# Kernel tuning notes

Measured on AMD Instinct MI355X. Metric: run time of the kernel, lower is better.

Reference implementation:

```python
import jax, jax.numpy as jnp
import numpy as np

B, N, F_IN, H, E = 8, 10000, 128, 128, 160000


def setup_inputs() -> dict:
    key = jax.random.key(0)
    ks = jax.random.split(key, 6)
    x = jax.random.normal(ks[0], (B, N, F_IN), dtype=jnp.float32)
    edge_index = jax.random.randint(ks[1], (2, E), 0, N, dtype=jnp.int64)
    # GCNConv params (glorot-ish scale), LayerNorm affine params
    W1 = jax.random.normal(ks[2], (F_IN, H), dtype=jnp.float32) / np.sqrt(F_IN)
    b1 = jnp.zeros((H,), dtype=jnp.float32)
    W2 = jax.random.normal(ks[3], (H, H), dtype=jnp.float32) / np.sqrt(H)
    b2 = jnp.zeros((H,), dtype=jnp.float32)
    ln_w = jnp.ones((H,), dtype=jnp.float32)
    ln_b = jnp.zeros((H,), dtype=jnp.float32)
    return {"x": x, "edge_index": edge_index, "W1": W1, "b1": b1,
            "W2": W2, "b2": b2, "ln_w": ln_w, "ln_b": ln_b}


def reference(x, edge_index, W1, b1, W2, b2, ln_w, ln_b):
    # x: [B, N, F]; edge_index: [2, E] shared across batch (tiled per graph
    # in the original via node offsets -> equivalent to vmapping over batch).
    n = x.shape[1]
    loops = jnp.arange(n, dtype=edge_index.dtype)
    src = jnp.concatenate([edge_index[0], loops])  # add self-loops (GCNConv default)
    dst = jnp.concatenate([edge_index[1], loops])
    # symmetric degree normalization: deg over targets with self-loops
    deg = jax.ops.segment_sum(jnp.ones(dst.shape[0], dtype=x.dtype), dst, num_segments=n)
    dinv = jnp.where(deg > 0, jax.lax.rsqrt(deg), 0.0)
    w_e = dinv[src] * dinv[dst]  # [E+N] per-edge norm

    def gcn_agg(h):  # h: [B, N, H] -> gather, scale, scatter-add
        msg = h[:, src, :] * w_e[None, :, None]  # [B, E+N, H]
        return jax.vmap(lambda m: jax.ops.segment_sum(m, dst, num_segments=n))(msg)

    h1 = jax.nn.relu(gcn_agg(x @ W1) + b1)
    h2 = gcn_agg(h1 @ W2) + b2
    # LayerNorm over last dim (eps=1e-5, torch default)
    mu = jnp.mean(h2, axis=-1, keepdims=True)
    var = jnp.mean(jnp.square(h2 - mu), axis=-1, keepdims=True)
    out = (h2 - mu) * jax.lax.rsqrt(var + 1e-5) * ln_w + ln_b
    return out  # [B, N, H]
```

## Files before the change

kernel.cpp:

```cpp
#include <hip/hip_runtime.h>
#include <hip/hip_bf16.h>

#define NNODES 10000
#define NB 8
#define NF 128
#define NE 160000

typedef __attribute__((ext_vector_type(8))) short  short8;
typedef __attribute__((ext_vector_type(8))) unsigned short ushort8;
typedef __attribute__((ext_vector_type(4))) float  f32x4;

__device__ __forceinline__ unsigned short f2b(float f) {
    union { float f; unsigned u; } v; v.f = f;
    unsigned r = v.u + 0x7FFF + ((v.u >> 16) & 1);
    return (unsigned short)(r >> 16);
}
__device__ __forceinline__ float b2f(unsigned short h) {
    union { unsigned u; float f; } v; v.u = ((unsigned)h) << 16;
    return v.f;
}


__global__ void k_zero(int* __restrict__ cnt, int* __restrict__ fill) {
    int i = blockIdx.x * blockDim.x + threadIdx.x;
    if (i < NNODES) { cnt[i] = 0; fill[i] = 0; }
}

__global__ void k_count(const int* __restrict__ ei, int* __restrict__ cnt) {
    int e = blockIdx.x * blockDim.x + threadIdx.x;
    if (e < NE) atomicAdd(&cnt[ei[NE + e]], 1);
}

__global__ void k_dinv(const int* __restrict__ cnt, float* __restrict__ dinv) {
    int i = blockIdx.x * blockDim.x + threadIdx.x;
    if (i < NNODES) dinv[i] = rsqrtf((float)(cnt[i] + 1));
}

__global__ void k_scan(const int* __restrict__ cnt, int* __restrict__ row_ptr) {
    __shared__ int part[1024];
    int t = threadIdx.x;
    const int CH = (NNODES + 1023) / 1024;
    int lo = t * CH, hi = min(lo + CH, NNODES);
    int s = 0;
    for (int i = lo; i < hi; i++) s += cnt[i];
    part[t] = s;
    __syncthreads();
    for (int off = 1; off < 1024; off <<= 1) {
        int v = (t >= off) ? part[t - off] : 0;
        __syncthreads();
        part[t] += v;
        __syncthreads();
    }
    int base = part[t] - s;
    for (int i = lo; i < hi; i++) { row_ptr[i] = base; base += cnt[i]; }
    if (t == 1023) row_ptr[NNODES] = part[1023];
}

__global__ void k_scatter(const int* __restrict__ ei, const int* __restrict__ row_ptr,
                          int* __restrict__ fill, const float* __restrict__ dinv,
                          int* __restrict__ col, float* __restrict__ wgt) {
    int e = blockIdx.x * blockDim.x + threadIdx.x;
    if (e >= NE) return;
    int s = ei[e];
    int d = ei[NE + e];
    int pos = row_ptr[d] + atomicAdd(&fill[d], 1);
    col[pos] = s;
    wgt[pos] = dinv[s] * dinv[d];
}

__global__ void k_wt(const float* __restrict__ W, unsigned short* __restrict__ Wt) {
    int id = blockIdx.x * 256 + threadIdx.x;
    int n = id >> 7, k = id & 127;
    Wt[(size_t)n * 128 + k] = f2b(W[(size_t)k * 128 + n]);
}

template <bool ABF16>
__global__ __launch_bounds__(256) void k_mm_mfma(const void* __restrict__ Ap,
                                                 const unsigned short* __restrict__ Wt,
                                                 unsigned short* __restrict__ Cn) {
    __shared__ unsigned short wlds[128 * 136];
    const int t = threadIdx.x;
    {
        const int r = t >> 1, h = t & 1;
        const ushort8* src = (const ushort8*)(Wt + r * 128 + h * 64);
        #pragma unroll
        for (int i = 0; i < 8; i++)
            *(ushort8*)(wlds + r * 136 + h * 64 + i * 8) = src[i];
    }
    __syncthreads();

    const int wid = t >> 6, lane = t & 63;
    const int quad = lane >> 4, l16 = lane & 15;
    const int m0 = blockIdx.x * 64 + (wid & 1) * 32;
    const int nb = (wid >> 1) * 64;
    const int kq = quad * 8;

    f32x4 acc[2][4] = {};

    #pragma unroll
    for (int ks = 0; ks < 128; ks += 32) {
        short8 bf[2];
        #pragma unroll
        for (int mi = 0; mi < 2; mi++) {
            const size_t row = (size_t)(m0 + mi * 16 + l16);
            if constexpr (ABF16) {
                bf[mi] = *(const short8*)((const unsigned short*)Ap + row * 128 + ks + kq);
            } else {
                const float* p = (const float*)Ap + row * 128 + ks + kq;
                float4 u0 = *(const float4*)p;
                float4 u1 = *(const float4*)(p + 4);
                short8 v;
                v[0] = (short)f2b(u0.x); v[1] = (short)f2b(u0.y);
                v[2] = (short)f2b(u0.z); v[3] = (short)f2b(u0.w);
                v[4] = (short)f2b(u1.x); v[5] = (short)f2b(u1.y);
                v[6] = (short)f2b(u1.z); v[7] = (short)f2b(u1.w);
                bf[mi] = v;
            }
        }
        short8 af[4];
        #pragma unroll
        for (int ni = 0; ni < 4; ni++)
            af[ni] = *(const short8*)(wlds + (nb + ni * 16 + l16) * 136 + ks + kq);
        #pragma unroll
        for (int mi = 0; mi < 2; mi++)
            #pragma unroll
            for (int ni = 0; ni < 4; ni++)
                acc[mi][ni] = __builtin_amdgcn_mfma_f32_16x16x32_bf16(
                    af[ni], bf[mi], acc[mi][ni], 0, 0, 0);
    }

    #pragma unroll
    for (int mi = 0; mi < 2; mi++) {
        int gm = m0 + mi * 16 + l16;
        int b = gm / NNODES;
        int n = gm - b * NNODES;
        unsigned short* dst = Cn + ((size_t)n * NB + b) * 128 + nb + quad * 4;
        #pragma unroll
        for (int ni = 0; ni < 4; ni++) {
            ushort4 o;
            o.x = f2b(acc[mi][ni][0]); o.y = f2b(acc[mi][ni][1]);
            o.z = f2b(acc[mi][ni][2]); o.w = f2b(acc[mi][ni][3]);
            *(ushort4*)(dst + ni * 16) = o;
        }
    }
}


__global__ __launch_bounds__(128) void k_agg_relu(const unsigned short* __restrict__ hN,
                                                  const float* __restrict__ bias,
                                                  const int* __restrict__ row_ptr,
                                                  const int* __restrict__ col,
                                                  const float* __restrict__ wgt,
                                                  const float* __restrict__ dinv,
                                                  unsigned short* __restrict__ h1b) {
    const int n = blockIdx.x, t = threadIdx.x;
    const int b = t >> 4, f0 = (t & 15) * 8;

    float di = dinv[n];
    float wself = di * di;
    float acc[8];
    {
        ushort8 u = *(const ushort8*)(hN + ((size_t)n * NB + b) * 128 + f0);
        #pragma unroll
        for (int i = 0; i < 8; i++) acc[i] = b2f(u[i]) * wself;
    }
    int e = row_ptr[n], e1 = row_ptr[n + 1];
    for (; e + 4 <= e1; e += 4) {
        int s0 = col[e], s1 = col[e + 1], s2 = col[e + 2], s3 = col[e + 3];
        float w0 = wgt[e], w1 = wgt[e + 1], w2 = wgt[e + 2], w3 = wgt[e + 3];
        ushort8 u0 = *(const ushort8*)(hN + ((size_t)s0 * NB + b) * 128 + f0);
        ushort8 u1 = *(const ushort8*)(hN + ((size_t)s1 * NB + b) * 128 + f0);
        ushort8 u2 = *(const ushort8*)(hN + ((size_t)s2 * NB + b) * 128 + f0);
        ushort8 u3 = *(const ushort8*)(hN + ((size_t)s3 * NB + b) * 128 + f0);
        #pragma unroll
        for (int i = 0; i < 8; i++) {
            acc[i] = fmaf(b2f(u0[i]), w0, acc[i]);
            acc[i] = fmaf(b2f(u1[i]), w1, acc[i]);
            acc[i] = fmaf(b2f(u2[i]), w2, acc[i]);
            acc[i] = fmaf(b2f(u3[i]), w3, acc[i]);
        }
    }
    for (; e < e1; ++e) {
        int s = col[e]; float w = wgt[e];
        ushort8 u = *(const ushort8*)(hN + ((size_t)s * NB + b) * 128 + f0);
        #pragma unroll
        for (int i = 0; i < 8; i++) acc[i] = fmaf(b2f(u[i]), w, acc[i]);
    }
    ushort8 o;
    #pragma unroll
    for (int i = 0; i < 8; i++)
        o[i] = f2b(fmaxf(acc[i] + bias[f0 + i], 0.f));
    *(ushort8*)(h1b + ((size_t)b * NNODES + n) * 128 + f0) = o;
}

__global__ __launch_bounds__(128) void k_agg_ln(const unsigned short* __restrict__ hN,
                                                const float* __restrict__ bias,
                                                const int* __restrict__ row_ptr,
                                                const int* __restrict__ col,
                                                const float* __restrict__ wgt,
                                                const float* __restrict__ dinv,
                                                const float* __restrict__ ln_w,
                                                const float* __restrict__ ln_b,
                                                float* __restrict__ out) {
    const int n = blockIdx.x, t = threadIdx.x;
    const int b = t >> 4, f0 = (t & 15) * 8;

    float di = dinv[n];
    float wself = di * di;
    float acc[8];
    {
        ushort8 u = *(const ushort8*)(hN + ((size_t)n * NB + b) * 128 + f0);
        #pragma unroll
        for (int i = 0; i < 8; i++) acc[i] = b2f(u[i]) * wself;
    }
    int e = row_ptr[n], e1 = row_ptr[n + 1];
    for (; e + 4 <= e1; e += 4) {
        int s0 = col[e], s1 = col[e + 1], s2 = col[e + 2], s3 = col[e + 3];
        float w0 = wgt[e], w1 = wgt[e + 1], w2 = wgt[e + 2], w3 = wgt[e + 3];
        ushort8 u0 = *(const ushort8*)(hN + ((size_t)s0 * NB + b) * 128 + f0);
        ushort8 u1 = *(const ushort8*)(hN + ((size_t)s1 * NB + b) * 128 + f0);
        ushort8 u2 = *(const ushort8*)(hN + ((size_t)s2 * NB + b) * 128 + f0);
        ushort8 u3 = *(const ushort8*)(hN + ((size_t)s3 * NB + b) * 128 + f0);
        #pragma unroll
        for (int i = 0; i < 8; i++) {
            acc[i] = fmaf(b2f(u0[i]), w0, acc[i]);
            acc[i] = fmaf(b2f(u1[i]), w1, acc[i]);
            acc[i] = fmaf(b2f(u2[i]), w2, acc[i]);
            acc[i] = fmaf(b2f(u3[i]), w3, acc[i]);
        }
    }
    for (; e < e1; ++e) {
        int s = col[e]; float w = wgt[e];
        ushort8 u = *(const ushort8*)(hN + ((size_t)s * NB + b) * 128 + f0);
        #pragma unroll
        for (int i = 0; i < 8; i++) acc[i] = fmaf(b2f(u[i]), w, acc[i]);
    }
    #pragma unroll
    for (int i = 0; i < 8; i++) acc[i] += bias[f0 + i];

    float s1 = 0.f, s2 = 0.f;
    #pragma unroll
    for (int i = 0; i < 8; i++) { s1 += acc[i]; s2 += acc[i] * acc[i]; }
    #pragma unroll
    for (int m = 1; m < 16; m <<= 1) {
        s1 += __shfl_xor(s1, m);
        s2 += __shfl_xor(s2, m);
    }
    float mu = s1 * (1.f / NF);
    float var = s2 * (1.f / NF) - mu * mu;
    float rs = rsqrtf(var + 1e-5f);

    float* dst = out + ((size_t)b * NNODES + n) * 128 + f0;
    float4 o0, o1;
    o0.x = (acc[0] - mu) * rs * ln_w[f0 + 0] + ln_b[f0 + 0];
    o0.y = (acc[1] - mu) * rs * ln_w[f0 + 1] + ln_b[f0 + 1];
    o0.z = (acc[2] - mu) * rs * ln_w[f0 + 2] + ln_b[f0 + 2];
    o0.w = (acc[3] - mu) * rs * ln_w[f0 + 3] + ln_b[f0 + 3];
    o1.x = (acc[4] - mu) * rs * ln_w[f0 + 4] + ln_b[f0 + 4];
    o1.y = (acc[5] - mu) * rs * ln_w[f0 + 5] + ln_b[f0 + 5];
    o1.z = (acc[6] - mu) * rs * ln_w[f0 + 6] + ln_b[f0 + 6];
    o1.w = (acc[7] - mu) * rs * ln_w[f0 + 7] + ln_b[f0 + 7];
    *(float4*)dst = o0;
    *(float4*)(dst + 4) = o1;
}


extern "C" void kernel_launch(void* const* d_in, const int* in_sizes, int n_in,
                              void* d_out, int out_size, void* d_ws, size_t ws_size,
                              hipStream_t stream) {
    const float* x    = (const float*)d_in[0];
    const int*   ei   = (const int*)d_in[1];
    const float* W1   = (const float*)d_in[2];
    const float* b1   = (const float*)d_in[3];
    const float* W2   = (const float*)d_in[4];
    const float* b2   = (const float*)d_in[5];
    const float* ln_w = (const float*)d_in[6];
    const float* ln_b = (const float*)d_in[7];
    float* out = (float*)d_out;

    char* ws = (char*)d_ws;
    int*            cnt     = (int*)(ws + 0);
    int*            fill    = (int*)(ws + 40192);
    int*            row_ptr = (int*)(ws + 80384);
    float*          dinv    = (float*)(ws + 120832);
    int*            col     = (int*)(ws + 161024);
    float*          wgt     = (float*)(ws + 801024);
    unsigned short* hA16    = (unsigned short*)(ws + 1441024);
    unsigned short* h1b     = (unsigned short*)(ws + 21921024);
    unsigned short* Wt1     = (unsigned short*)cnt;
    unsigned short* Wt2     = (unsigned short*)fill;

    k_zero   <<<(NNODES + 255) / 256, 256, 0, stream>>>(cnt, fill);
    k_count  <<<(NE + 255) / 256, 256, 0, stream>>>(ei, cnt);
    k_dinv   <<<(NNODES + 255) / 256, 256, 0, stream>>>(cnt, dinv);
    k_scan   <<<1, 1024, 0, stream>>>(cnt, row_ptr);
    k_scatter<<<(NE + 255) / 256, 256, 0, stream>>>(ei, row_ptr, fill, dinv, col, wgt);

    k_wt<<<64, 256, 0, stream>>>(W1, Wt1);
    k_wt<<<64, 256, 0, stream>>>(W2, Wt2);

    k_mm_mfma<false><<<(NB * NNODES) / 64, 256, 0, stream>>>(x, Wt1, hA16);
    k_agg_relu<<<NNODES, 128, 0, stream>>>(hA16, b1, row_ptr, col, wgt, dinv, h1b);

    k_mm_mfma<true><<<(NB * NNODES) / 64, 256, 0, stream>>>(h1b, Wt2, hA16);
    k_agg_ln<<<NNODES, 128, 0, stream>>>(hA16, b2, row_ptr, col, wgt, dinv, ln_w, ln_b, out);
}
```

Baseline: 260.8 us.

## Remap aggregation to one wavefront per node-batch and stage GEMM output via LDS

The aggregation kernels now assign one 64-lane wavefront per (node, batch) pair, with each lane owning two features. Each neighbor gather therefore becomes a single contiguous 256-byte row read by the wave, and the LayerNorm reduction is a full-wave shuffle. Blocks are ordered batch-fastest, so neighboring blocks touch the same node rows. The MFMA GEMM epilogue now stages its bf16 tile in LDS so each row is written with wide contiguous stores, and outputs use nontemporal stores. The cost is more blocks, more gather instructions per lane with fewer bytes each, and an extra LDS round trip with two barriers in the GEMM.

```diff
diff --git a/kernel.cpp b/kernel.cpp
--- a/kernel.cpp
+++ b/kernel.cpp
@@ -18,6 +18,12 @@
 __device__ __forceinline__ float b2f(unsigned short h) {
     union { unsigned u; float f; } v; v.u = ((unsigned)h) << 16;
     return v.f;
+}
+__device__ __forceinline__ float b2f_lo(unsigned u) {
+    union { unsigned u; float f; } v; v.u = u << 16; return v.f;
+}
+__device__ __forceinline__ float b2f_hi(unsigned u) {
+    union { unsigned u; float f; } v; v.u = u & 0xffff0000u; return v.f;
 }
 
 
@@ -129,71 +135,82 @@
                     af[ni], bf[mi], acc[mi][ni], 0, 0, 0);
     }
 
-    #pragma unroll
-    for (int mi = 0; mi < 2; mi++) {
-        int gm = m0 + mi * 16 + l16;
+    __syncthreads();
+    {
+        const int rbase = (wid & 1) * 32;
+        #pragma unroll
+        for (int mi = 0; mi < 2; mi++) {
+            int rr = rbase + mi * 16 + l16;
+            #pragma unroll
+            for (int ni = 0; ni < 4; ni++) {
+                ushort4 o;
+                o.x = f2b(acc[mi][ni][0]); o.y = f2b(acc[mi][ni][1]);
+                o.z = f2b(acc[mi][ni][2]); o.w = f2b(acc[mi][ni][3]);
+                *(ushort4*)(wlds + rr * 136 + nb + ni * 16 + quad * 4) = o;
+            }
+        }
+    }
+    __syncthreads();
+    {
+        const int r = t >> 2, seg = t & 3;
+        int gm = blockIdx.x * 64 + r;
         int b = gm / NNODES;
         int n = gm - b * NNODES;
-        unsigned short* dst = Cn + ((size_t)n * NB + b) * 128 + nb + quad * 4;
-        #pragma unroll
-        for (int ni = 0; ni < 4; ni++) {
-            ushort4 o;
-            o.x = f2b(acc[mi][ni][0]); o.y = f2b(acc[mi][ni][1]);
-            o.z = f2b(acc[mi][ni][2]); o.w = f2b(acc[mi][ni][3]);
-            *(ushort4*)(dst + ni * 16) = o;
-        }
-    }
-}
-
-
-__global__ __launch_bounds__(128) void k_agg_relu(const unsigned short* __restrict__ hN,
+        unsigned short* dst = Cn + ((size_t)n * NB + b) * 128 + seg * 32;
+        const unsigned short* srow = wlds + r * 136 + seg * 32;
+        #pragma unroll
+        for (int i = 0; i < 4; i++)
+            *(ushort8*)(dst + i * 8) = *(const ushort8*)(srow + i * 8);
+    }
+}
+
+
+__global__ __launch_bounds__(256) void k_agg_relu(const unsigned int* __restrict__ hNu,
                                                   const float* __restrict__ bias,
                                                   const int* __restrict__ row_ptr,
                                                   const int* __restrict__ col,
                                                   const float* __restrict__ wgt,
                                                   const float* __restrict__ dinv,
-                                                  unsigned short* __restrict__ h1b) {
-    const int n = blockIdx.x, t = threadIdx.x;
-    const int b = t >> 4, f0 = (t & 15) * 8;
-
+                                                  unsigned int* __restrict__ h1u) {
+    const int t = threadIdx.x;
+    const int b = blockIdx.x & 7;
+    const int g = blockIdx.x >> 3;
+    const int wid = __builtin_amdgcn_readfirstlane(t >> 6);
+    const int lane = t & 63;
+    const int n = g * 4 + wid;
+
+    const unsigned int* base = hNu + (size_t)b * 64 + lane;
     float di = dinv[n];
     float wself = di * di;
-    float acc[8];
-    {
-        ushort8 u = *(const ushort8*)(hN + ((size_t)n * NB + b) * 128 + f0);
-        #pragma unroll
-        for (int i = 0; i < 8; i++) acc[i] = b2f(u[i]) * wself;
-    }
+    unsigned int u = base[(size_t)n * 512];
+    float a0 = b2f_lo(u) * wself;
+    float a1 = b2f_hi(u) * wself;
+
     int e = row_ptr[n], e1 = row_ptr[n + 1];
     for (; e + 4 <= e1; e += 4) {
         int s0 = col[e], s1 = col[e + 1], s2 = col[e + 2], s3 = col[e + 3];
         float w0 = wgt[e], w1 = wgt[e + 1], w2 = wgt[e + 2], w3 = wgt[e + 3];
-        ushort8 u0 = *(const ushort8*)(hN + ((size_t)s0 * NB + b) * 128 + f0);
-        ushort8 u1 = *(const ushort8*)(hN + ((size_t)s1 * NB + b) * 128 + f0);
-        ushort8 u2 = *(const ushort8*)(hN + ((size_t)s2 * NB + b) * 128 + f0);
-        ushort8 u3 = *(const ushort8*)(hN + ((size_t)s3 * NB + b) * 128 + f0);
-        #pragma unroll
-        for (int i = 0; i < 8; i++) {
-            acc[i] = fmaf(b2f(u0[i]), w0, acc[i]);
-            acc[i] = fmaf(b2f(u1[i]), w1, acc[i]);
-            acc[i] = fmaf(b2f(u2[i]), w2, acc[i]);
-            acc[i] = fmaf(b2f(u3[i]), w3, acc[i]);
-        }
+        unsigned int u0 = base[(size_t)s0 * 512];
+        unsigned int u1 = base[(size_t)s1 * 512];
+        unsigned int u2 = base[(size_t)s2 * 512];
+        unsigned int u3 = base[(size_t)s3 * 512];
+        a0 = fmaf(b2f_lo(u0), w0, a0); a1 = fmaf(b2f_hi(u0), w0, a1);
+        a0 = fmaf(b2f_lo(u1), w1, a0); a1 = fmaf(b2f_hi(u1), w1, a1);
+        a0 = fmaf(b2f_lo(u2), w2, a0); a1 = fmaf(b2f_hi(u2), w2, a1);
+        a0 = fmaf(b2f_lo(u3), w3, a0); a1 = fmaf(b2f_hi(u3), w3, a1);
     }
     for (; e < e1; ++e) {
         int s = col[e]; float w = wgt[e];
-        ushort8 u = *(const ushort8*)(hN + ((size_t)s * NB + b) * 128 + f0);
-        #pragma unroll
-        for (int i = 0; i < 8; i++) acc[i] = fmaf(b2f(u[i]), w, acc[i]);
-    }
-    ushort8 o;
-    #pragma unroll
-    for (int i = 0; i < 8; i++)
-        o[i] = f2b(fmaxf(acc[i] + bias[f0 + i], 0.f));
-    *(ushort8*)(h1b + ((size_t)b * NNODES + n) * 128 + f0) = o;
-}
-
-__global__ __launch_bounds__(128) void k_agg_ln(const unsigned short* __restrict__ hN,
+        unsigned int uu = base[(size_t)s * 512];
+        a0 = fmaf(b2f_lo(uu), w, a0); a1 = fmaf(b2f_hi(uu), w, a1);
+    }
+    a0 = fmaxf(a0 + bias[lane * 2], 0.f);
+    a1 = fmaxf(a1 + bias[lane * 2 + 1], 0.f);
+    unsigned int o = (unsigned int)f2b(a0) | ((unsigned int)f2b(a1) << 16);
+    __builtin_nontemporal_store(o, &h1u[((size_t)b * NNODES + n) * 64 + lane]);
+}
+
+__global__ __launch_bounds__(256) void k_agg_ln(const unsigned int* __restrict__ hNu,
                                                 const float* __restrict__ bias,
                                                 const int* __restrict__ row_ptr,
                                                 const int* __restrict__ col,
@@ -202,47 +219,45 @@
                                                 const float* __restrict__ ln_w,
                                                 const float* __restrict__ ln_b,
                                                 float* __restrict__ out) {
-    const int n = blockIdx.x, t = threadIdx.x;
-    const int b = t >> 4, f0 = (t & 15) * 8;
-
+    const int t = threadIdx.x;
+    const int b = blockIdx.x & 7;
+    const int g = blockIdx.x >> 3;
+    const int wid = __builtin_amdgcn_readfirstlane(t >> 6);
+    const int lane = t & 63;
+    const int n = g * 4 + wid;
+
+    const unsigned int* base = hNu + (size_t)b * 64 + lane;
     float di = dinv[n];
     float wself = di * di;
-    float acc[8];
-    {
-        ushort8 u = *(const ushort8*)(hN + ((size_t)n * NB + b) * 128 + f0);
-        #pragma unroll
-        for (int i = 0; i < 8; i++) acc[i] = b2f(u[i]) * wself;
-    }
+    unsigned int u = base[(size_t)n * 512];
+    float a0 = b2f_lo(u) * wself;
+    float a1 = b2f_hi(u) * wself;
+
     int e = row_ptr[n], e1 = row_ptr[n + 1];
     for (; e + 4 <= e1; e += 4) {
         int s0 = col[e], s1 = col[e + 1], s2 = col[e + 2], s3 = col[e + 3];
         float w0 = wgt[e], w1 = wgt[e + 1], w2 = wgt[e + 2], w3 = wgt[e + 3];
-        ushort8 u0 = *(const ushort8*)(hN + ((size_t)s0 * NB + b) * 128 + f0);
-        ushort8 u1 = *(const ushort8*)(hN + ((size_t)s1 * NB + b) * 128 + f0);
-        ushort8 u2 = *(const ushort8*)(hN + ((size_t)s2 * NB + b) * 128 + f0);
-        ushort8 u3 = *(const ushort8*)(hN + ((size_t)s3 * NB + b) * 128 + f0);
-        #pragma unroll
-        for (int i = 0; i < 8; i++) {
-            acc[i] = fmaf(b2f(u0[i]), w0, acc[i]);
-            acc[i] = fmaf(b2f(u1[i]), w1, acc[i]);
-            acc[i] = fmaf(b2f(u2[i]), w2, acc[i]);
-            acc[i] = fmaf(b2f(u3[i]), w3, acc[i]);
-        }
+        unsigned int u0 = base[(size_t)s0 * 512];
+        unsigned int u1 = base[(size_t)s1 * 512];
+        unsigned int u2 = base[(size_t)s2 * 512];
+        unsigned int u3 = base[(size_t)s3 * 512];
+        a0 = fmaf(b2f_lo(u0), w0, a0); a1 = fmaf(b2f_hi(u0), w0, a1);
+        a0 = fmaf(b2f_lo(u1), w1, a0); a1 = fmaf(b2f_hi(u1), w1, a1);
+        a0 = fmaf(b2f_lo(u2), w2, a0); a1 = fmaf(b2f_hi(u2), w2, a1);
+        a0 = fmaf(b2f_lo(u3), w3, a0); a1 = fmaf(b2f_hi(u3), w3, a1);
     }
     for (; e < e1; ++e) {
         int s = col[e]; float w = wgt[e];
-        ushort8 u = *(const ushort8*)(hN + ((size_t)s * NB + b) * 128 + f0);
-        #pragma unroll
-        for (int i = 0; i < 8; i++) acc[i] = fmaf(b2f(u[i]), w, acc[i]);
-    }
+        unsigned int uu = base[(size_t)s * 512];
+        a0 = fmaf(b2f_lo(uu), w, a0); a1 = fmaf(b2f_hi(uu), w, a1);
+    }
+    a0 += bias[lane * 2];
+    a1 += bias[lane * 2 + 1];
+
+    float s1 = a0 + a1;
+    float s2 = a0 * a0 + a1 * a1;
     #pragma unroll
-    for (int i = 0; i < 8; i++) acc[i] += bias[f0 + i];
-
-    float s1 = 0.f, s2 = 0.f;
-    #pragma unroll
-    for (int i = 0; i < 8; i++) { s1 += acc[i]; s2 += acc[i] * acc[i]; }
-    #pragma unroll
-    for (int m = 1; m < 16; m <<= 1) {
+    for (int m = 1; m < 64; m <<= 1) {
         s1 += __shfl_xor(s1, m);
         s2 += __shfl_xor(s2, m);
     }
@@ -250,18 +265,11 @@
     float var = s2 * (1.f / NF) - mu * mu;
     float rs = rsqrtf(var + 1e-5f);
 
-    float* dst = out + ((size_t)b * NNODES + n) * 128 + f0;
-    float4 o0, o1;
-    o0.x = (acc[0] - mu) * rs * ln_w[f0 + 0] + ln_b[f0 + 0];
-    o0.y = (acc[1] - mu) * rs * ln_w[f0 + 1] + ln_b[f0 + 1];
-    o0.z = (acc[2] - mu) * rs * ln_w[f0 + 2] + ln_b[f0 + 2];
-    o0.w = (acc[3] - mu) * rs * ln_w[f0 + 3] + ln_b[f0 + 3];
-    o1.x = (acc[4] - mu) * rs * ln_w[f0 + 4] + ln_b[f0 + 4];
-    o1.y = (acc[5] - mu) * rs * ln_w[f0 + 5] + ln_b[f0 + 5];
-    o1.z = (acc[6] - mu) * rs * ln_w[f0 + 6] + ln_b[f0 + 6];
-    o1.w = (acc[7] - mu) * rs * ln_w[f0 + 7] + ln_b[f0 + 7];
-    *(float4*)dst = o0;
-    *(float4*)(dst + 4) = o1;
+    float o0 = (a0 - mu) * rs * ln_w[lane * 2] + ln_b[lane * 2];
+    float o1 = (a1 - mu) * rs * ln_w[lane * 2 + 1] + ln_b[lane * 2 + 1];
+    float* dst = out + ((size_t)b * NNODES + n) * 128 + lane * 2;
+    __builtin_nontemporal_store(o0, dst);
+    __builtin_nontemporal_store(o1, dst + 1);
 }
 
 
@@ -300,8 +308,12 @@
     k_wt<<<64, 256, 0, stream>>>(W2, Wt2);
 
     k_mm_mfma<false><<<(NB * NNODES) / 64, 256, 0, stream>>>(x, Wt1, hA16);
-    k_agg_relu<<<NNODES, 128, 0, stream>>>(hA16, b1, row_ptr, col, wgt, dinv, h1b);
+    k_agg_relu<<<(NNODES / 4) * NB, 256, 0, stream>>>((const unsigned int*)hA16, b1,
+                                                      row_ptr, col, wgt, dinv,
+                                                      (unsigned int*)h1b);
 
     k_mm_mfma<true><<<(NB * NNODES) / 64, 256, 0, stream>>>(h1b, Wt2, hA16);
-    k_agg_ln<<<NNODES, 128, 0, stream>>>(hA16, b2, row_ptr, col, wgt, dinv, ln_w, ln_b, out);
-}
+    k_agg_ln<<<(NNODES / 4) * NB, 256, 0, stream>>>((const unsigned int*)hA16, b2,
+                                                    row_ptr, col, wgt, dinv,
+                                                    ln_w, ln_b, out);
+}
```

New measurement: 240.0 us. -8.0%, faster.
